# Performance work log

Hardware: AMD Instinct MI355X
Metric: run time of the kernel (lower is better)

## Reference

```python
import jax, jax.numpy as jnp
import numpy as np

C_M, C_Z, C, H = 256, 128, 32, 8
EPS = 1e-5

def _ln(x, g, b):
    mu = jnp.mean(x, axis=-1, keepdims=True)
    var = jnp.var(x, axis=-1, keepdims=True)
    return (x - mu) * jax.lax.rsqrt(var + EPS) * g + b

def setup_inputs() -> dict:
    key = jax.random.key(0)
    ks = jax.random.split(key, 12)
    s = 0.02
    return {
        "m": jax.random.normal(ks[0], (128, 384, C_M), jnp.float32),
        "z": jax.random.normal(ks[1], (384, 384, C_Z), jnp.float32),
        "ln_m_g": jnp.ones((C_M,), jnp.float32),
        "ln_m_b": jnp.zeros((C_M,), jnp.float32),
        "ln_z_g": jnp.ones((C_Z,), jnp.float32),
        "ln_z_b": jnp.zeros((C_Z,), jnp.float32),
        "Wq": jax.random.normal(ks[2], (C_M, H, C), jnp.float32) * s,
        "Wk": jax.random.normal(ks[3], (C_M, H, C), jnp.float32) * s,
        "Wv": jax.random.normal(ks[4], (C_M, H, C), jnp.float32) * s,
        "Wb": jax.random.normal(ks[5], (C_Z, H), jnp.float32) * s,
        "Wg": jax.random.normal(ks[6], (C_M, H, C), jnp.float32) * s,
        "bg": jnp.ones((H, C), jnp.float32),
        "Wo": jax.random.normal(ks[7], (H, C, C_M), jnp.float32) * s,
        "bo": jnp.zeros((C_M,), jnp.float32),
    }

def reference(m, z, ln_m_g, ln_m_b, ln_z_g, ln_z_b, Wq, Wk, Wv, Wb, Wg, bg, Wo, bo):
    # Algorithm 7: MSA row-wise gated self-attention with pair bias.
    mn = _ln(m, ln_m_g, ln_m_b)                      # (S, R, c_m)
    zn = _ln(z, ln_z_g, ln_z_b)                      # (R, R, c_z)
    b = jnp.einsum('qkz,zh->hqk', zn, Wb)            # per-head pair bias (H, R, R)
    q = jnp.einsum('srm,mhc->shrc', mn, Wq)          # (S, H, R, C)
    k = jnp.einsum('srm,mhc->shrc', mn, Wk)
    v = jnp.einsum('srm,mhc->shrc', mn, Wv)
    logits = jnp.einsum('shqc,shkc->shqk', q, k) * (1.0 / np.sqrt(C)) + b[None]
    a = jax.nn.softmax(logits, axis=-1)              # (S, H, Rq, Rk)
    o = jnp.einsum('shqk,shkc->sqhc', a, v)          # (S, R, H, C)
    g = jax.nn.sigmoid(jnp.einsum('srm,mhc->srhc', mn, Wg) + bg)
    o = g * o
    out = jnp.einsum('srhc,hcm->srm', o, Wo) + bo    # (S, R, c_m)
    return out
```

## Files before the change

kernel.cpp:

```cpp
#include <hip/hip_runtime.h>
#include <hip/hip_bf16.h>

#define DEVINL __device__ __forceinline__

typedef __attribute__((ext_vector_type(8))) short bf16x8;
typedef __attribute__((ext_vector_type(4))) float f32x4;

DEVINL float bf2f(unsigned short u) {
    unsigned int v = ((unsigned int)u) << 16;
    return __builtin_bit_cast(float, v);
}
DEVINL unsigned short f2bf(float f) {
    unsigned int u = __builtin_bit_cast(unsigned int, f);
    u = (u + 0x7FFFu + ((u >> 16) & 1u)) >> 16;
    return (unsigned short)u;
}
DEVINL float wave_sum(float v) {
#pragma unroll
    for (int off = 32; off > 0; off >>= 1) v += __shfl_xor(v, off, 64);
    return v;
}
DEVINL void gload16(const void* g, void* l) {
    __builtin_amdgcn_global_load_lds(
        (const __attribute__((address_space(1))) void*)g,
        (__attribute__((address_space(3))) void*)l, 16, 0, 0);
}


__global__ __launch_bounds__(256) void k_ln_m(const float* __restrict__ m,
                                              const float* __restrict__ gm,
                                              const float* __restrict__ bm,
                                              unsigned short* __restrict__ mn) {
    const int lane = threadIdx.x & 63;
    const int row  = (blockIdx.x << 2) + (threadIdx.x >> 6);
    const float4 x = *(const float4*)(m + (size_t)row * 256 + lane * 4);
    float s  = x.x + x.y + x.z + x.w;
    float s2 = x.x * x.x + x.y * x.y + x.z * x.z + x.w * x.w;
    s = wave_sum(s); s2 = wave_sum(s2);
    const float mean = s * (1.f / 256.f);
    const float var  = s2 * (1.f / 256.f) - mean * mean;
    const float rstd = rsqrtf(var + 1e-5f);
    const float4 g = *(const float4*)(gm + lane * 4);
    const float4 b = *(const float4*)(bm + lane * 4);
    ushort4 o;
    o.x = f2bf((x.x - mean) * rstd * g.x + b.x);
    o.y = f2bf((x.y - mean) * rstd * g.y + b.y);
    o.z = f2bf((x.z - mean) * rstd * g.z + b.z);
    o.w = f2bf((x.w - mean) * rstd * g.w + b.w);
    *(ushort4*)(mn + (size_t)row * 256 + lane * 4) = o;
}

__global__ __launch_bounds__(64) void k_prep_wb(const float* __restrict__ gz,
                                                const float* __restrict__ bz,
                                                const float* __restrict__ Wb,
                                                float* __restrict__ W2,
                                                float* __restrict__ SK) {
    const int lane = threadIdx.x;
    const float LOG2E = 1.4426950408889634f;
    float sC[8], sK[8];
#pragma unroll
    for (int h = 0; h < 8; h++) { sC[h] = 0.f; sK[h] = 0.f; }
#pragma unroll
    for (int i = 0; i < 2; i++) {
        const int c = lane + i * 64;
        const float g = gz[c] * LOG2E, b = bz[c] * LOG2E;
        const float4 w0 = *(const float4*)(Wb + c * 8);
        const float4 w1 = *(const float4*)(Wb + c * 8 + 4);
        const float w[8] = {w0.x, w0.y, w0.z, w0.w, w1.x, w1.y, w1.z, w1.w};
        float wg[8];
#pragma unroll
        for (int h = 0; h < 8; h++) {
            wg[h] = g * w[h];
            sC[h] += wg[h];
            sK[h] += b * w[h];
        }
        float4 o0 = {wg[0], wg[1], wg[2], wg[3]};
        float4 o1 = {wg[4], wg[5], wg[6], wg[7]};
        *(float4*)(W2 + c * 8)     = o0;
        *(float4*)(W2 + c * 8 + 4) = o1;
    }
#pragma unroll
    for (int h = 0; h < 8; h++) { sC[h] = wave_sum(sC[h]); sK[h] = wave_sum(sK[h]); }
    if (lane == 0) {
#pragma unroll
        for (int h = 0; h < 8; h++) { SK[h] = sC[h]; SK[8 + h] = sK[h]; }
    }
}

__global__ __launch_bounds__(256) void k_ln_z_bias(const float* __restrict__ z,
                                                   const float* __restrict__ W2,
                                                   const float* __restrict__ SK,
                                                   float* __restrict__ bT) {
    const int tid  = threadIdx.x;
    const int lane = tid & 63;
    const int id   = lane & 31;
    const int wave = tid >> 6;
    const int p = blockIdx.x * 8 + wave * 2 + (lane >> 5);

    float w[4][8];
#pragma unroll
    for (int cc = 0; cc < 4; cc++) {
        const float4 a = *(const float4*)(W2 + (id * 4 + cc) * 8);
        const float4 b = *(const float4*)(W2 + (id * 4 + cc) * 8 + 4);
        w[cc][0] = a.x; w[cc][1] = a.y; w[cc][2] = a.z; w[cc][3] = a.w;
        w[cc][4] = b.x; w[cc][5] = b.y; w[cc][6] = b.z; w[cc][7] = b.w;
    }

    const float4 zv = *(const float4*)(z + (size_t)p * 128 + id * 4);
    float s  = zv.x + zv.y + zv.z + zv.w;
    float s2 = zv.x * zv.x + zv.y * zv.y + zv.z * zv.z + zv.w * zv.w;
    float d[8];
#pragma unroll
    for (int h = 0; h < 8; h++)
        d[h] = zv.x * w[0][h] + zv.y * w[1][h] + zv.z * w[2][h] + zv.w * w[3][h];

#pragma unroll
    for (int off = 1; off <= 16; off <<= 1) {
        s  += __shfl_xor(s,  off, 64);
        s2 += __shfl_xor(s2, off, 64);
    }
    const float mean = s * (1.f / 128.f);
    const float var  = s2 * (1.f / 128.f) - mean * mean;
    const float rstd = rsqrtf(var + 1e-5f);

    const int b0 = id & 1;
    {
        float t0 = b0 ? d[0] : d[4], k0 = b0 ? d[4] : d[0];
        float t1 = b0 ? d[1] : d[5], k1 = b0 ? d[5] : d[1];
        float t2 = b0 ? d[2] : d[6], k2 = b0 ? d[6] : d[2];
        float t3 = b0 ? d[3] : d[7], k3 = b0 ? d[7] : d[3];
        d[0] = k0 + __shfl_xor(t0, 1, 64);
        d[1] = k1 + __shfl_xor(t1, 1, 64);
        d[2] = k2 + __shfl_xor(t2, 1, 64);
        d[3] = k3 + __shfl_xor(t3, 1, 64);
    }
    const int b1 = (id >> 1) & 1;
    {
        float u0 = b1 ? d[0] : d[2], m0 = b1 ? d[2] : d[0];
        float u1 = b1 ? d[1] : d[3], m1 = b1 ? d[3] : d[1];
        d[0] = m0 + __shfl_xor(u0, 2, 64);
        d[1] = m1 + __shfl_xor(u1, 2, 64);
    }
    const int b2 = (id >> 2) & 1;
    float D;
    {
        float u = b2 ? d[0] : d[1], m = b2 ? d[1] : d[0];
        D = m + __shfl_xor(u, 4, 64);
    }
    D += __shfl_xor(D, 8, 64);
    D += __shfl_xor(D, 16, 64);

    const int h = ((id & 1) << 2) | (id & 2) | ((id >> 2) & 1);
    const float bias = rstd * (D - mean * SK[h]) + SK[8 + h];
    if (id < 8) {
        const int q  = p / 384;
        const int kk = p - q * 384;
        const int kb = kk >> 5, kk5 = kk & 31;
        const size_t o = ((size_t)((kb * 2 + ((kk5 >> 2) & 1)) * 4 + (kk5 >> 3)) * 384 + q) * 4 + (kk5 & 3);
        bT[(size_t)h * 147456 + o] = bias;
    }
}

__global__ __launch_bounds__(256) void k_prep(const float* __restrict__ S,
                                              unsigned short* __restrict__ D) {
    __shared__ float T[64][68];
    const int k0 = blockIdx.x * 64, n0 = blockIdx.y * 64;
    const int tr = threadIdx.x >> 4, tc4 = (threadIdx.x & 15) * 4;
#pragma unroll
    for (int i = 0; i < 4; i++) {
        const int k = i * 16 + tr;
        const float4 v = *(const float4*)(S + (size_t)(k0 + k) * 256 + n0 + tc4);
        T[k][tc4 + 0] = v.x; T[k][tc4 + 1] = v.y; T[k][tc4 + 2] = v.z; T[k][tc4 + 3] = v.w;
    }
    __syncthreads();
#pragma unroll
    for (int i = 0; i < 4; i++) {
        const int n = i * 16 + tr;
        ushort4 o;
        o.x = f2bf(T[tc4 + 0][n]);
        o.y = f2bf(T[tc4 + 1][n]);
        o.z = f2bf(T[tc4 + 2][n]);
        o.w = f2bf(T[tc4 + 3][n]);
        *(ushort4*)(D + (size_t)(n0 + n) * 256 + k0 + tc4) = o;
    }
}

template<int MODE>
__global__ __launch_bounds__(256) void k_gemm(const unsigned short* __restrict__ A,
                                              const unsigned short* __restrict__ BT,
                                              const float* __restrict__ bias,
                                              unsigned short* __restrict__ o0,
                                              unsigned short* __restrict__ o1,
                                              unsigned short* __restrict__ o2,
                                              unsigned short* __restrict__ o3,
                                              float* __restrict__ fout) {
    __shared__ unsigned short As[8192];
    __shared__ unsigned short Bs[8192];
    const int tid = threadIdx.x;
    const int w = tid >> 6, lane = tid & 63;
    const int col = lane & 15, quad = lane >> 4;
    const int wm = w >> 1, wn = w & 1;
    const int R0 = blockIdx.x * 128;
    const int N0 = blockIdx.y * 128;

    f32x4 acc[4][4];
#pragma unroll
    for (int i = 0; i < 4; i++)
#pragma unroll
        for (int j = 0; j < 4; j++) acc[i][j] = (f32x4){0.f, 0.f, 0.f, 0.f};

    const unsigned short* Ag = A  + (size_t)R0 * 256;
    const unsigned short* Bg = BT + (size_t)N0 * 256;

    for (int ks = 0; ks < 4; ks++) {
        if (ks) __syncthreads();
        const int k0 = ks * 64;
#pragma unroll
        for (int it = 0; it < 4; it++) {
            const int cb = it * 256 + w * 64;
            const int chunk = cb + lane;
            const int row = chunk >> 3;
            const int ch  = (chunk & 7) ^ (row & 7);
            gload16(Ag + (size_t)row * 256 + k0 + ch * 8, As + (size_t)cb * 8);
            gload16(Bg + (size_t)row * 256 + k0 + ch * 8, Bs + (size_t)cb * 8);
        }
        __syncthreads();
#pragma unroll
        for (int ksub = 0; ksub < 2; ksub++) {
            const int c = ksub * 4 + quad;
            bf16x8 Af[4], Bf[4];
#pragma unroll
            for (int mt = 0; mt < 4; mt++) {
                const int r = wm * 64 + mt * 16 + col;
                Af[mt] = *(const bf16x8*)(As + r * 64 + (c ^ (r & 7)) * 8);
            }
#pragma unroll
            for (int nt = 0; nt < 4; nt++) {
                const int r = wn * 64 + nt * 16 + col;
                Bf[nt] = *(const bf16x8*)(Bs + r * 64 + (c ^ (r & 7)) * 8);
            }
#pragma unroll
            for (int mt = 0; mt < 4; mt++)
#pragma unroll
                for (int nt = 0; nt < 4; nt++)
                    acc[mt][nt] = __builtin_amdgcn_mfma_f32_16x16x32_bf16(Af[mt], Bf[nt], acc[mt][nt], 0, 0, 0);
        }
    }

    if (MODE == 0) {
        const int mat = blockIdx.y >> 1;
        const int s = R0 / 384;
        const int rbase = R0 - s * 384;
        const int n0r = (blockIdx.y & 1) * 128;
        if (mat == 1 || mat == 2) {
            unsigned short* outp = (mat == 1) ? o1 : o2;
#pragma unroll
            for (int nt = 0; nt < 4; nt++) {
                const int hc = n0r + wn * 64 + nt * 16 + col;
                const int h = hc >> 5, cc = hc & 31;
                unsigned short* op = outp + (size_t)(s * 8 + h) * 12288;
                if (mat == 1) {
#pragma unroll
                    for (int mt = 0; mt < 4; mt++) {
                        const int r2 = rbase + wm * 64 + mt * 16 + quad * 4;
                        const int ab = (r2 >> 5) * 1024 + ((r2 >> 2) & 1) * 512
                                     + ((r2 & 31) >> 3) * 128 + cc;
#pragma unroll
                        for (int rr = 0; rr < 4; rr++)
                            op[ab + rr * 32] = f2bf(acc[mt][nt][rr]);
                    }
                } else {
                    unsigned short* opv = op + (cc >> 4) * 512 + (cc & 15) * 32;
#pragma unroll
                    for (int mt = 0; mt < 4; mt++) {
                        const int r2 = rbase + wm * 64 + mt * 16 + quad * 4;
                        ushort4 o;
                        o.x = f2bf(acc[mt][nt][0]);
                        o.y = f2bf(acc[mt][nt][1]);
                        o.z = f2bf(acc[mt][nt][2]);
                        o.w = f2bf(acc[mt][nt][3]);
                        *(ushort4*)(opv + (r2 >> 5) * 1024 + (r2 & 31)) = o;
                    }
                }
            }
        } else {
            unsigned short* outp = (mat == 0) ? o0 : o3;
#pragma unroll
            for (int nt = 0; nt < 4; nt++) {
                const int hc = n0r + wn * 64 + nt * 16 + col;
                const int h = hc >> 5, cc = hc & 31;
                const float bgv = bias[hc];
                unsigned short* op = outp + (size_t)(s * 8 + h) * 384 * 32 + cc;
#pragma unroll
                for (int mt = 0; mt < 4; mt++) {
                    const int r2 = rbase + wm * 64 + mt * 16 + quad * 4;
#pragma unroll
                    for (int rr = 0; rr < 4; rr++) {
                        float v = acc[mt][nt][rr];
                        v = (mat == 3) ? 1.f / (1.f + __expf(-(v + bgv)))
                                       : v * 0.25507788224f;
                        op[(size_t)(r2 + rr) * 32] = f2bf(v);
                    }
                }
            }
        }
    } else {
#pragma unroll
        for (int nt = 0; nt < 4; nt++) {
            const int n = N0 + wn * 64 + nt * 16 + col;
            const float bov = bias[n];
            float* op = fout + n;
#pragma unroll
            for (int mt = 0; mt < 4; mt++) {
                const int r2 = R0 + wm * 64 + mt * 16 + quad * 4;
#pragma unroll
                for (int rr = 0; rr < 4; rr++)
                    op[(size_t)(r2 + rr) * 256] = acc[mt][nt][rr] + bov;
            }
        }
    }
}

__global__ __launch_bounds__(256) void k_attn(const unsigned short* __restrict__ qw,
                                              const unsigned short* __restrict__ kf,
                                              const unsigned short* __restrict__ vf,
                                              const unsigned short* __restrict__ gw,
                                              const float* __restrict__ bT,
                                              unsigned short* __restrict__ og) {
    const int s = blockIdx.x & 127;
    const int h = blockIdx.x >> 7;
    const int tid  = threadIdx.x;
    const int wave = tid >> 6;
    const int lane = tid & 63;
    const int col  = lane & 15;
    const int quad = lane >> 4;
    const size_t base = ((size_t)(s * 8 + h)) * 12288;
    const float* bTh = bT + (size_t)h * 147456;

    const int qbase = wave * 96;
    bf16x8 Qf[6];
#pragma unroll
    for (int qt = 0; qt < 6; qt++)
        Qf[qt] = *(const bf16x8*)(qw + base + (size_t)(qbase + qt * 16 + col) * 32 + quad * 8);

    f32x4 OT0[6], OT1[6];
    float lsum[6];
#pragma unroll
    for (int qt = 0; qt < 6; qt++) {
        OT0[qt] = (f32x4){0.f, 0.f, 0.f, 0.f};
        OT1[qt] = (f32x4){0.f, 0.f, 0.f, 0.f};
        lsum[qt] = 0.f;
    }

    const unsigned short* kwb = kf + base + col * 32 + quad * 8;
    const unsigned short* vtb = vf + base + col * 32 + quad * 8;

    for (int kb = 0; kb < 12; kb++) {
        const bf16x8 Kf0 = *(const bf16x8*)(kwb + kb * 1024);
        const bf16x8 Kf1 = *(const bf16x8*)(kwb + kb * 1024 + 512);
        const bf16x8 VA0 = *(const bf16x8*)(vtb + kb * 1024);
        const bf16x8 VA1 = *(const bf16x8*)(vtb + kb * 1024 + 512);
#pragma unroll
        for (int qt = 0; qt < 6; qt++) {
            const int q = qbase + qt * 16 + col;
            const float4 b0 = *(const float4*)(bTh + ((size_t)(kb * 8 + quad) * 384 + q) * 4);
            const float4 b1 = *(const float4*)(bTh + ((size_t)(kb * 8 + 4 + quad) * 384 + q) * 4);
            const f32x4 c0 = {b0.x, b0.y, b0.z, b0.w};
            const f32x4 c1 = {b1.x, b1.y, b1.z, b1.w};
            const f32x4 St0 = __builtin_amdgcn_mfma_f32_16x16x32_bf16(Kf0, Qf[qt], c0, 0, 0, 0);
            const f32x4 St1 = __builtin_amdgcn_mfma_f32_16x16x32_bf16(Kf1, Qf[qt], c1, 0, 0, 0);
            float p0[4], p1[4];
            p0[0] = exp2f(St0[0]);
            p0[1] = exp2f(St0[1]);
            p0[2] = exp2f(St0[2]);
            p0[3] = exp2f(St0[3]);
            p1[0] = exp2f(St1[0]);
            p1[1] = exp2f(St1[1]);
            p1[2] = exp2f(St1[2]);
            p1[3] = exp2f(St1[3]);
            lsum[qt] += (p0[0] + p0[1]) + (p0[2] + p0[3]) + (p1[0] + p1[1]) + (p1[2] + p1[3]);
            union { bf16x8 v; __hip_bfloat162 h2[4]; } U;
            U.h2[0] = __float22bfloat162_rn(make_float2(p0[0], p0[1]));
            U.h2[1] = __float22bfloat162_rn(make_float2(p0[2], p0[3]));
            U.h2[2] = __float22bfloat162_rn(make_float2(p1[0], p1[1]));
            U.h2[3] = __float22bfloat162_rn(make_float2(p1[2], p1[3]));
            OT0[qt] = __builtin_amdgcn_mfma_f32_16x16x32_bf16(VA0, U.v, OT0[qt], 0, 0, 0);
            OT1[qt] = __builtin_amdgcn_mfma_f32_16x16x32_bf16(VA1, U.v, OT1[qt], 0, 0, 0);
        }
    }

#pragma unroll
    for (int qt = 0; qt < 6; qt++) {
        float l = lsum[qt];
        l += __shfl_xor(l, 16, 64);
        l += __shfl_xor(l, 32, 64);
        const float inv = 1.f / l;
        const int q = qbase + qt * 16 + col;
        const ushort4 g0 = *(const ushort4*)(gw + base + (size_t)q * 32 + quad * 4);
        const ushort4 g1 = *(const ushort4*)(gw + base + (size_t)q * 32 + quad * 4 + 16);
        ushort4 o0s, o1s;
        o0s.x = f2bf(OT0[qt][0] * inv * bf2f(g0.x));
        o0s.y = f2bf(OT0[qt][1] * inv * bf2f(g0.y));
        o0s.z = f2bf(OT0[qt][2] * inv * bf2f(g0.z));
        o0s.w = f2bf(OT0[qt][3] * inv * bf2f(g0.w));
        o1s.x = f2bf(OT1[qt][0] * inv * bf2f(g1.x));
        o1s.y = f2bf(OT1[qt][1] * inv * bf2f(g1.y));
        o1s.z = f2bf(OT1[qt][2] * inv * bf2f(g1.z));
        o1s.w = f2bf(OT1[qt][3] * inv * bf2f(g1.w));
        unsigned short* op = og + ((size_t)s * 384 + q) * 256 + h * 32 + quad * 4;
        *(ushort4*)(op)      = o0s;
        *(ushort4*)(op + 16) = o1s;
    }
}

extern "C" void kernel_launch(void* const* d_in, const int* in_sizes, int n_in,
                              void* d_out, int out_size, void* d_ws, size_t ws_size,
                              hipStream_t stream) {
    const float* m   = (const float*)d_in[0];
    const float* z   = (const float*)d_in[1];
    const float* lmg = (const float*)d_in[2];
    const float* lmb = (const float*)d_in[3];
    const float* lzg = (const float*)d_in[4];
    const float* lzb = (const float*)d_in[5];
    const float* Wq  = (const float*)d_in[6];
    const float* Wk  = (const float*)d_in[7];
    const float* Wv  = (const float*)d_in[8];
    const float* Wb  = (const float*)d_in[9];
    const float* Wg  = (const float*)d_in[10];
    const float* bg  = (const float*)d_in[11];
    const float* Wo  = (const float*)d_in[12];
    const float* bo  = (const float*)d_in[13];
    float* out = (float*)d_out;

    char* ws = (char*)d_ws;
    unsigned short* mn  = (unsigned short*)(ws);
    float*          bT  = (float*)(ws + 25165824);
    unsigned short* qw  = (unsigned short*)(ws + 29884416);
    unsigned short* kw  = (unsigned short*)(ws + 55050240);
    unsigned short* vw  = (unsigned short*)(ws + 80216064);
    unsigned short* gw  = (unsigned short*)(ws + 105381888);
    unsigned short* ogp = (unsigned short*)(ws + 130547712);
    unsigned short* WTp = (unsigned short*)d_out;
    float*          W2  = (float*)((char*)d_out + (1 << 20));
    float*          SKt = (float*)((char*)d_out + (1 << 20) + 4096);
    unsigned short* WoT = (unsigned short*)(ws + 25165824);

    k_prep<<<dim3(4, 4), 256, 0, stream>>>(Wq, WTp + 0 * 65536);
    k_prep<<<dim3(4, 4), 256, 0, stream>>>(Wk, WTp + 1 * 65536);
    k_prep<<<dim3(4, 4), 256, 0, stream>>>(Wv, WTp + 2 * 65536);
    k_prep<<<dim3(4, 4), 256, 0, stream>>>(Wg, WTp + 3 * 65536);
    k_prep_wb<<<dim3(1), 64, 0, stream>>>(lzg, lzb, Wb, W2, SKt);
    k_ln_m<<<dim3(12288), 256, 0, stream>>>(m, lmg, lmb, mn);
    k_ln_z_bias<<<dim3(18432), 256, 0, stream>>>(z, W2, SKt, bT);
    k_gemm<0><<<dim3(384, 8), 256, 0, stream>>>(mn, WTp, bg, qw, kw, vw, gw, nullptr);
    k_attn<<<dim3(1024), 256, 0, stream>>>(qw, kw, vw, gw, bT, ogp);
    k_prep<<<dim3(4, 4), 256, 0, stream>>>(Wo, WoT);
    k_gemm<1><<<dim3(384, 2), 256, 0, stream>>>(ogp, WoT, bo, nullptr, nullptr, nullptr, nullptr, out);
}
```

Baseline: 405.4 us.

## Split attention query rows across two blocks, batch weight prep, use native exp2

The attention kernel now launches twice as many blocks, each handling half the query rows with three query tiles per wave instead of six. This is meant to raise occupancy and cut register pressure. Bias loads for each key block are hoisted ahead of the MFMAs, and exp2f is replaced with the hardware exp2 builtin. The four weight transposes are merged into one launch, and the Wo prep moves before attention so WoT can live in the freed mn region. The cost is that each K/V tile is now loaded by twice as many blocks.

New measurement: 355.5 us. -12.3%, faster.

```diff
diff --git a/kernel.cpp b/kernel.cpp
--- a/kernel.cpp
+++ b/kernel.cpp
@@ -185,6 +185,36 @@
     }
 }
 
+__global__ __launch_bounds__(256) void k_prep4(const float* __restrict__ Wq,
+                                               const float* __restrict__ Wk,
+                                               const float* __restrict__ Wv,
+                                               const float* __restrict__ Wg,
+                                               unsigned short* __restrict__ D) {
+    __shared__ float T[64][68];
+    const int zz = blockIdx.z;
+    const float* S = (zz == 0) ? Wq : (zz == 1) ? Wk : (zz == 2) ? Wv : Wg;
+    unsigned short* Dz = D + (size_t)zz * 65536;
+    const int k0 = blockIdx.x * 64, n0 = blockIdx.y * 64;
+    const int tr = threadIdx.x >> 4, tc4 = (threadIdx.x & 15) * 4;
+#pragma unroll
+    for (int i = 0; i < 4; i++) {
+        const int k = i * 16 + tr;
+        const float4 v = *(const float4*)(S + (size_t)(k0 + k) * 256 + n0 + tc4);
+        T[k][tc4 + 0] = v.x; T[k][tc4 + 1] = v.y; T[k][tc4 + 2] = v.z; T[k][tc4 + 3] = v.w;
+    }
+    __syncthreads();
+#pragma unroll
+    for (int i = 0; i < 4; i++) {
+        const int n = i * 16 + tr;
+        ushort4 o;
+        o.x = f2bf(T[tc4 + 0][n]);
+        o.y = f2bf(T[tc4 + 1][n]);
+        o.z = f2bf(T[tc4 + 2][n]);
+        o.w = f2bf(T[tc4 + 3][n]);
+        *(ushort4*)(Dz + (size_t)(n0 + n) * 256 + k0 + tc4) = o;
+    }
+}
+
 template<int MODE>
 __global__ __launch_bounds__(256) void k_gemm(const unsigned short* __restrict__ A,
                                               const unsigned short* __restrict__ BT,
@@ -327,26 +357,26 @@
                                               const unsigned short* __restrict__ gw,
                                               const float* __restrict__ bT,
                                               unsigned short* __restrict__ og) {
-    const int s = blockIdx.x & 127;
-    const int h = blockIdx.x >> 7;
+    const int s    = blockIdx.x & 127;
+    const int half = (blockIdx.x >> 7) & 1;
+    const int h    = blockIdx.x >> 8;
     const int tid  = threadIdx.x;
     const int wave = tid >> 6;
     const int lane = tid & 63;
     const int col  = lane & 15;
     const int quad = lane >> 4;
     const size_t base = ((size_t)(s * 8 + h)) * 12288;
-    const float* bTh = bT + (size_t)h * 147456;
-
-    const int qbase = wave * 96;
-    bf16x8 Qf[6];
-#pragma unroll
-    for (int qt = 0; qt < 6; qt++)
+    const int qbase = half * 192 + wave * 48;
+
+    bf16x8 Qf[3];
+#pragma unroll
+    for (int qt = 0; qt < 3; qt++)
         Qf[qt] = *(const bf16x8*)(qw + base + (size_t)(qbase + qt * 16 + col) * 32 + quad * 8);
 
-    f32x4 OT0[6], OT1[6];
-    float lsum[6];
-#pragma unroll
-    for (int qt = 0; qt < 6; qt++) {
+    f32x4 OT0[3], OT1[3];
+    float lsum[3];
+#pragma unroll
+    for (int qt = 0; qt < 3; qt++) {
         OT0[qt] = (f32x4){0.f, 0.f, 0.f, 0.f};
         OT1[qt] = (f32x4){0.f, 0.f, 0.f, 0.f};
         lsum[qt] = 0.f;
@@ -354,30 +384,36 @@
 
     const unsigned short* kwb = kf + base + col * 32 + quad * 8;
     const unsigned short* vtb = vf + base + col * 32 + quad * 8;
+    const float* bp = bT + (size_t)h * 147456 + ((size_t)quad * 384 + qbase + col) * 4;
 
     for (int kb = 0; kb < 12; kb++) {
-        const bf16x8 Kf0 = *(const bf16x8*)(kwb + kb * 1024);
-        const bf16x8 Kf1 = *(const bf16x8*)(kwb + kb * 1024 + 512);
-        const bf16x8 VA0 = *(const bf16x8*)(vtb + kb * 1024);
-        const bf16x8 VA1 = *(const bf16x8*)(vtb + kb * 1024 + 512);
-#pragma unroll
-        for (int qt = 0; qt < 6; qt++) {
-            const int q = qbase + qt * 16 + col;
-            const float4 b0 = *(const float4*)(bTh + ((size_t)(kb * 8 + quad) * 384 + q) * 4);
-            const float4 b1 = *(const float4*)(bTh + ((size_t)(kb * 8 + 4 + quad) * 384 + q) * 4);
-            const f32x4 c0 = {b0.x, b0.y, b0.z, b0.w};
-            const f32x4 c1 = {b1.x, b1.y, b1.z, b1.w};
-            const f32x4 St0 = __builtin_amdgcn_mfma_f32_16x16x32_bf16(Kf0, Qf[qt], c0, 0, 0, 0);
-            const f32x4 St1 = __builtin_amdgcn_mfma_f32_16x16x32_bf16(Kf1, Qf[qt], c1, 0, 0, 0);
+        const bf16x8 Kf0 = *(const bf16x8*)(kwb);
+        const bf16x8 Kf1 = *(const bf16x8*)(kwb + 512);
+        const bf16x8 VA0 = *(const bf16x8*)(vtb);
+        const bf16x8 VA1 = *(const bf16x8*)(vtb + 512);
+        kwb += 1024; vtb += 1024;
+        f32x4 B0[3], B1[3];
+#pragma unroll
+        for (int qt = 0; qt < 3; qt++) {
+            const float4 a = *(const float4*)(bp + qt * 64);
+            const float4 b = *(const float4*)(bp + 6144 + qt * 64);
+            B0[qt] = (f32x4){a.x, a.y, a.z, a.w};
+            B1[qt] = (f32x4){b.x, b.y, b.z, b.w};
+        }
+        bp += 12288;
+#pragma unroll
+        for (int qt = 0; qt < 3; qt++) {
+            const f32x4 St0 = __builtin_amdgcn_mfma_f32_16x16x32_bf16(Kf0, Qf[qt], B0[qt], 0, 0, 0);
+            const f32x4 St1 = __builtin_amdgcn_mfma_f32_16x16x32_bf16(Kf1, Qf[qt], B1[qt], 0, 0, 0);
             float p0[4], p1[4];
-            p0[0] = exp2f(St0[0]);
-            p0[1] = exp2f(St0[1]);
-            p0[2] = exp2f(St0[2]);
-            p0[3] = exp2f(St0[3]);
-            p1[0] = exp2f(St1[0]);
-            p1[1] = exp2f(St1[1]);
-            p1[2] = exp2f(St1[2]);
-            p1[3] = exp2f(St1[3]);
+            p0[0] = __builtin_amdgcn_exp2f(St0[0]);
+            p0[1] = __builtin_amdgcn_exp2f(St0[1]);
+            p0[2] = __builtin_amdgcn_exp2f(St0[2]);
+            p0[3] = __builtin_amdgcn_exp2f(St0[3]);
+            p1[0] = __builtin_amdgcn_exp2f(St1[0]);
+            p1[1] = __builtin_amdgcn_exp2f(St1[1]);
+            p1[2] = __builtin_amdgcn_exp2f(St1[2]);
+            p1[3] = __builtin_amdgcn_exp2f(St1[3]);
             lsum[qt] += (p0[0] + p0[1]) + (p0[2] + p0[3]) + (p1[0] + p1[1]) + (p1[2] + p1[3]);
             union { bf16x8 v; __hip_bfloat162 h2[4]; } U;
             U.h2[0] = __float22bfloat162_rn(make_float2(p0[0], p0[1]));
@@ -390,7 +426,7 @@
     }
 
 #pragma unroll
-    for (int qt = 0; qt < 6; qt++) {
+    for (int qt = 0; qt < 3; qt++) {
         float l = lsum[qt];
         l += __shfl_xor(l, 16, 64);
         l += __shfl_xor(l, 32, 64);
@@ -441,19 +477,16 @@
     unsigned short* gw  = (unsigned short*)(ws + 105381888);
     unsigned short* ogp = (unsigned short*)(ws + 130547712);
     unsigned short* WTp = (unsigned short*)d_out;
-    float*          W2  = (float*)((char*)d_out + (1 << 20));
+    float*          W2s = (float*)((char*)d_out + (1 << 20));
     float*          SKt = (float*)((char*)d_out + (1 << 20) + 4096);
-    unsigned short* WoT = (unsigned short*)(ws + 25165824);
-
-    k_prep<<<dim3(4, 4), 256, 0, stream>>>(Wq, WTp + 0 * 65536);
-    k_prep<<<dim3(4, 4), 256, 0, stream>>>(Wk, WTp + 1 * 65536);
-    k_prep<<<dim3(4, 4), 256, 0, stream>>>(Wv, WTp + 2 * 65536);
-    k_prep<<<dim3(4, 4), 256, 0, stream>>>(Wg, WTp + 3 * 65536);
-    k_prep_wb<<<dim3(1), 64, 0, stream>>>(lzg, lzb, Wb, W2, SKt);
+    unsigned short* WoT = (unsigned short*)(ws);
+
+    k_prep4<<<dim3(4, 4, 4), 256, 0, stream>>>(Wq, Wk, Wv, Wg, WTp);
+    k_prep_wb<<<dim3(1), 64, 0, stream>>>(lzg, lzb, Wb, W2s, SKt);
     k_ln_m<<<dim3(12288), 256, 0, stream>>>(m, lmg, lmb, mn);
-    k_ln_z_bias<<<dim3(18432), 256, 0, stream>>>(z, W2, SKt, bT);
+    k_ln_z_bias<<<dim3(18432), 256, 0, stream>>>(z, W2s, SKt, bT);
     k_gemm<0><<<dim3(384, 8), 256, 0, stream>>>(mn, WTp, bg, qw, kw, vw, gw, nullptr);
-    k_attn<<<dim3(1024), 256, 0, stream>>>(qw, kw, vw, gw, bT, ogp);
     k_prep<<<dim3(4, 4), 256, 0, stream>>>(Wo, WoT);
+    k_attn<<<dim3(2048), 256, 0, stream>>>(qw, kw, vw, gw, bT, ogp);
     k_gemm<1><<<dim3(384, 2), 256, 0, stream>>>(ogp, WoT, bo, nullptr, nullptr, nullptr, nullptr, out);
 }
```
